# Kernel tuning notes

Hardware: AMD Instinct MI355X
Metric: run time of the kernel (lower is better)

The kernel has to match this reference:

```python
import jax, jax.numpy as jnp
import numpy as np

B, C, H, W = 8, 256, 128, 128


def setup_inputs() -> dict:
    key = jax.random.key(0)
    ks = jax.random.split(key, 8)
    s = 1.0 / np.sqrt(C)
    return {
        "edge_feature": jax.random.normal(ks[0], (B, C, H, W), jnp.float32),
        "mask_feature": jax.random.normal(ks[1], (B, C, H, W), jnp.float32),
        # 1x1 conv weights [out_dim, in_dim] + biases
        "Wq": jax.random.normal(ks[2], (C, C), jnp.float32) * s,
        "bq": jax.random.normal(ks[3], (C,), jnp.float32) * 0.01,
        "Wk": jax.random.normal(ks[4], (C, C), jnp.float32) * s,
        "bk": jax.random.normal(ks[5], (C,), jnp.float32) * 0.01,
        "Wv": jax.random.normal(ks[6], (C, C), jnp.float32) * s,
        "bv": jax.random.normal(ks[7], (C,), jnp.float32) * 0.01,
        # torch initializes gamma=0; use 0.5 so the attention path is exercised
        "gamma": jnp.array(0.5, jnp.float32),
    }


def _conv1x1(x, w, b):
    # x: [B,C,H,W], w: [O,C] -> [B,O,H,W]
    return jnp.einsum('oc,bchw->bohw', w, x) + b[None, :, None, None]


def reference(edge_feature, mask_feature, Wq, bq, Wk, bk, Wv, bv, gamma):
    b, c, h, w = edge_feature.shape
    q = _conv1x1(edge_feature, Wq, bq)
    k = _conv1x1(edge_feature, Wk, bk)
    v = _conv1x1(mask_feature, Wv, bv)

    # Criss-cross energies (note: source forward does NOT apply the INF diag mask)
    energy_H = jnp.einsum('bchw,bcjw->bhwj', q, k)  # [B,H,W,H] column attention
    energy_W = jnp.einsum('bchw,bchj->bhwj', q, k)  # [B,H,W,W] row attention

    att = jax.nn.softmax(jnp.concatenate([energy_H, energy_W], axis=3), axis=3)
    att_H4 = att[..., :h]   # [B,H,W,H]
    att_W4 = att[..., h:]   # [B,H,W,W]

    out_H = jnp.einsum('bcjw,bhwj->bchw', v, att_H4)
    out_W = jnp.einsum('bchj,bhwj->bchw', v, att_W4)
    out = gamma * (out_H + out_W) + mask_feature

    # Match torch's returned attention layouts: [B*W,H,H] and [B*H,W,W]
    att_H = jnp.transpose(att_H4, (0, 2, 1, 3)).reshape(b * w, h, h)
    att_W = att_W4.reshape(b * h, w, w)
    return (out, att_H, att_W)
```

## Files before the change

kernel.cpp:

```cpp
#include <hip/hip_runtime.h>

typedef unsigned short u16;
typedef unsigned int   u32;
typedef __attribute__((ext_vector_type(8))) short short8;
typedef __attribute__((ext_vector_type(4))) float f32x4;

#define HW_   16384
constexpr long CHW_ = 4194304L;
constexpr long NT   = 33554432L;

#define GLDS(g, l) __builtin_amdgcn_global_load_lds( \
    (const __attribute__((address_space(1))) void*)(g), \
    (__attribute__((address_space(3))) void*)(l), 16, 0, 0)

__device__ inline u16 f2bf(float x){ u32 u = __float_as_uint(x); u += 0x7fff + ((u>>16)&1); return (u16)(u>>16); }
__device__ inline float bf2f(u16 h){ return __uint_as_float(((u32)h)<<16); }

__device__ inline const short8* frg(const u16* T, int r, int c){
  return (const short8*)(T + r*64 + ((c ^ (r&7))<<3));
}


template<int MODE>
__global__ __launch_bounds__(256) void gemm_nt(
    const char* __restrict__ Aq, const char* __restrict__ Bq,
    const char* __restrict__ Aq2, const char* __restrict__ Bq2,
    const float* __restrict__ bias, const float* __restrict__ gammap,
    float* __restrict__ outFa, float* __restrict__ outFb,
    u16* __restrict__ outUa, u16* __restrict__ outUb)
{
  constexpr int NTl = (MODE <= 1) ? 8 : (MODE == 2 ? 4 : 2);
  __shared__ __align__(16) u16 smem[34048];

  const int t    = threadIdx.x;
  const int lane = t & 63;
  const int wid  = t >> 6;
  const int wr   = (wid >> 1) << 6;
  const int wc   = (wid & 1) << 6;

  long abase = 0, bbase = 0, ars = 0, brs = 0;
  int b = 0, m0 = 0, n0 = 0, xx = 0, ct = 0, dir = 0, sOut = 0;
  const char* Ause = Aq;
  const char* Buse = Bq;
  u16* outU = outUa;

  if constexpr (MODE == 0) {
    b = blockIdx.z; m0 = blockIdx.x << 7; n0 = blockIdx.y << 7;
    abase = ((long)b * HW_ + m0) * 1024; ars = 1024;
    bbase = (long)n0 * 1024;             brs = 1024;
  } else if constexpr (MODE == 1) {
    int bid = blockIdx.x;
    b = bid >> 8; dir = (bid >> 7) & 1; xx = bid & 127;
    sOut = b * 128 + xx;
    if (dir) { abase = (long)b * 16777216L + (long)xx * 1024; ars = 131072; }
    else     { abase = (long)b * 16777216L + (long)xx * 131072; ars = 1024; }
    bbase = abase; brs = ars;
  } else if constexpr (MODE == 2) {
    b = blockIdx.z; m0 = blockIdx.y << 7; n0 = blockIdx.x << 7;
    abase = (long)m0 * 512;              ars = 512;
    bbase = ((long)b * HW_ + n0) * 512;  brs = 512;
  } else {
    int s = blockIdx.x; ct = blockIdx.y; b = s >> 7; xx = s & 127;
    sOut = s;
    if (blockIdx.z) { Ause = Aq2; Buse = Bq2; outU = outUb; }
    abase = ((long)b * 256 + (long)(ct << 7)) * 32768L + (long)xx * 256; ars = 32768;
    bbase = (long)s * 32768L; brs = 256;
  }

  const char* pA = Ause + abase;
  const char* pB = Buse + bbase;

  f32x4 acc[4][4];
  for (int i = 0; i < 4; i++)
    for (int j = 0; j < 4; j++)
      acc[i][j] = (f32x4){0.f, 0.f, 0.f, 0.f};

  auto stage = [&](int buf, int kt) {
    u16* T1 = smem + buf * 17024;
    u16* T2 = T1 + 8192;
    const long ko = (long)kt * 128;
    #pragma unroll
    for (int i = 0; i < 4; i++) {
      int r = (i << 5) + (t >> 3);
      int c = (t & 7) ^ (r & 7);
      GLDS(pA + (long)r * ars + ko + (c << 4), T1 + (i << 11) + ((t >> 6) << 9));
      GLDS(pB + (long)r * brs + ko + (c << 4), T2 + (i << 11) + ((t >> 6) << 9));
    }
  };

  const int khi = lane >> 4;
  const int rl  = lane & 15;

  stage(0, 0);
  stage(1, 1);

  #pragma unroll
  for (int kt = 0; kt < NTl; ++kt) {
    if (kt + 1 < NTl) asm volatile("s_waitcnt vmcnt(8)" ::: "memory");
    else              asm volatile("s_waitcnt vmcnt(0)" ::: "memory");
    __builtin_amdgcn_sched_barrier(0);
    __builtin_amdgcn_s_barrier();
    __builtin_amdgcn_sched_barrier(0);

    const u16* T1 = smem + (kt & 1) * 17024;
    const u16* T2 = T1 + 8192;

    short8 fa0[4], fa1[4], fb0[4], fb1[4];
    #pragma unroll
    for (int f = 0; f < 4; f++) {
      fa0[f] = *frg(T1, wr + f * 16 + rl, khi);
      fa1[f] = *frg(T1, wr + f * 16 + rl, 4 + khi);
      fb0[f] = *frg(T2, wc + f * 16 + rl, khi);
      fb1[f] = *frg(T2, wc + f * 16 + rl, 4 + khi);
    }

    __builtin_amdgcn_s_setprio(1);
    #pragma unroll
    for (int fm = 0; fm < 4; fm++) {
      #pragma unroll
      for (int fn = 0; fn < 4; fn++) {
        if constexpr (MODE <= 1) {
          acc[fm][fn] = __builtin_amdgcn_mfma_f32_16x16x32_bf16(fa0[fm], fb0[fn], acc[fm][fn], 0, 0, 0);
          acc[fm][fn] = __builtin_amdgcn_mfma_f32_16x16x32_bf16(fa0[fm], fb1[fn], acc[fm][fn], 0, 0, 0);
          acc[fm][fn] = __builtin_amdgcn_mfma_f32_16x16x32_bf16(fa1[fm], fb0[fn], acc[fm][fn], 0, 0, 0);
        } else {
          acc[fm][fn] = __builtin_amdgcn_mfma_f32_16x16x32_bf16(fa0[fm], fb0[fn], acc[fm][fn], 0, 0, 0);
          acc[fm][fn] = __builtin_amdgcn_mfma_f32_16x16x32_bf16(fa1[fm], fb1[fn], acc[fm][fn], 0, 0, 0);
        }
      }
    }
    __builtin_amdgcn_s_setprio(0);

    __builtin_amdgcn_s_barrier();
    __builtin_amdgcn_sched_barrier(0);
    if (kt + 2 < NTl) stage(kt & 1, kt + 2);
  }

  float gma = 0.f;
  if constexpr (MODE == 3) gma = gammap[0];
  float* LDSE = (float*)smem;

  #pragma unroll
  for (int fm = 0; fm < 4; fm++) {
    #pragma unroll
    for (int fn = 0; fn < 4; fn++) {
      #pragma unroll
      for (int r = 0; r < 4; r++) {
        int lr = wr + fm * 16 + ((lane >> 4) << 2) + r;
        int lc = wc + fn * 16 + rl;
        float v = acc[fm][fn][r];
        if constexpr (MODE == 0) v += bias[n0 + lc];
        if constexpr (MODE == 2) v += bias[m0 + lr];
        if constexpr (MODE == 3) v *= gma;
        LDSE[lr * 132 + lc] = v;
      }
    }
  }
  __syncthreads();

  if constexpr (MODE == 0) {
    u16* outp = (n0 < 256) ? outUa : outUb;
    long rowb = ((long)b * HW_ + m0) * 512;
    int cbu = (n0 & 255) * 2;
    #pragma unroll
    for (int k = 0; k < 16; ++k) {
      int row = k * 8 + (t >> 5);
      int iu  = (t & 31) * 8;
      int off = iu & 63;
      int lcol = (iu >> 6) * 32 + (off & 31);
      const float* src = &LDSE[row * 132 + lcol];
      u16 o[8];
      if (off < 32) {
        #pragma unroll
        for (int j = 0; j < 8; j++) o[j] = f2bf(src[j]);
      } else {
        #pragma unroll
        for (int j = 0; j < 8; j++) { float v = src[j]; u16 h = f2bf(v); o[j] = f2bf(v - bf2f(h)); }
      }
      *(short8*)(outp + rowb + (long)row * 512 + cbu + iu) = *(short8*)o;
    }
  } else if constexpr (MODE == 1) {
    float* op = dir ? outFb : outFa;
    long ob = (long)sOut * 16384;
    #pragma unroll
    for (int k = 0; k < 16; ++k) {
      int row = k * 8 + (t >> 5);
      int c4 = (t & 31) * 4;
      f32x4 v = *(const f32x4*)&LDSE[row * 132 + c4];
      *(f32x4*)(op + ob + (long)row * 128 + c4) = v;
    }
  } else {
    #pragma unroll
    for (int k = 0; k < 8; ++k) {
      int row = k * 16 + (t >> 4);
      int c8 = (t & 15) * 8;
      const float* src = &LDSE[row * 132 + c8];
      u16 o[8];
      #pragma unroll
      for (int j = 0; j < 8; j++) o[j] = f2bf(src[j]);
      long addr;
      if constexpr (MODE == 2) addr = ((long)b * 256 + m0 + row) * HW_ + n0 + c8;
      else                     addr = ((long)b * 256 + (ct << 7) + row) * HW_ + (long)xx * 128 + c8;
      *(short8*)(outU + addr) = *(short8*)o;
    }
  }
}

__global__ __launch_bounds__(256) void split_transpose2(const float* __restrict__ edge,
    const float* __restrict__ mask, u16* __restrict__ Xs, u16* __restrict__ Mt)
{
  int b = blockIdx.z, c0 = blockIdx.y << 5, p0 = blockIdx.x << 5;
  __shared__ float tileE[32][33];
  __shared__ float tileM[32][33];
  int tx = threadIdx.x, ty = threadIdx.y;
  const float* E = edge + (long)b * CHW_;
  const float* M = mask + (long)b * CHW_;
  #pragma unroll
  for (int r = 0; r < 4; r++) {
    int cc = ty + (r << 3);
    long g = (long)(c0 + cc) * HW_ + p0 + tx;
    tileE[cc][tx] = E[g];
    tileM[cc][tx] = M[g];
  }
  __syncthreads();
  int blk = (c0 >> 5) * 64;
  #pragma unroll
  for (int r = 0; r < 4; r++) {
    int pp = ty + (r << 3);
    long prow = (long)b * HW_ + p0 + pp;
    float x = tileE[tx][pp];
    u16 h = f2bf(x);
    Xs[prow * 512 + blk + tx]      = h;
    Xs[prow * 512 + blk + 32 + tx] = f2bf(x - bf2f(h));
    Mt[prow * 256 + c0 + tx]       = f2bf(tileM[tx][pp]);
  }
}

__global__ __launch_bounds__(256) void wsplit(const float* __restrict__ Wq,
    const float* __restrict__ Wk, const float* __restrict__ Wv,
    const float* __restrict__ bq, const float* __restrict__ bk,
    u16* Wc, u16* Wvp, float* bcat)
{
  int i = blockIdx.x * 256 + threadIdx.x;
  int o = i >> 8, c = i & 255;
  long pos = (long)o * 512 + (c >> 5) * 64 + (c & 31);
  float q = Wq[i]; u16 a = f2bf(q); Wc[pos] = a; Wc[pos + 32] = f2bf(q - bf2f(a));
  float k = Wk[i]; u16 d = f2bf(k);
  Wc[pos + 131072] = d; Wc[pos + 131072 + 32] = f2bf(k - bf2f(d));
  Wvp[i] = f2bf(Wv[i]);
  if (blockIdx.x == 0) {
    bcat[threadIdx.x]       = bq[threadIdx.x];
    bcat[256 + threadIdx.x] = bk[threadIdx.x];
  }
}

__global__ __launch_bounds__(256) void transpose_hw_bf16(const u16* __restrict__ src,
                                                         u16* __restrict__ dst)
{
  int bc = blockIdx.z;
  int h0 = blockIdx.x << 5, w0 = blockIdx.y << 5;
  long base = (long)bc * HW_;
  __shared__ u16 tile[32][34];
  int tx = threadIdx.x, ty = threadIdx.y;
  #pragma unroll
  for (int r = 0; r < 4; r++)
    tile[ty + (r << 3)][tx] = src[base + (long)(h0 + ty + (r << 3)) * 128 + w0 + tx];
  __syncthreads();
  #pragma unroll
  for (int r = 0; r < 4; r++) {
    int ww = ty + (r << 3);
    dst[base + (long)(w0 + ww) * 128 + h0 + tx] = tile[tx][ww];
  }
}

__global__ __launch_bounds__(256) void softmax_kernel(float* __restrict__ attH,
    float* __restrict__ attW, u16* __restrict__ aHb, u16* __restrict__ aWb)
{
  int g  = threadIdx.x & 31;
  long r = (long)blockIdx.x * 8 + (threadIdx.x >> 5);
  int b = (int)(r >> 14);
  int h = (int)((r >> 7) & 127);
  int w = (int)(r & 127);
  long baseH = ((long)(b * 128 + w) * 128 + h) * 128;
  long baseW = r * 128;
  float* rp = (g < 16) ? (attH + baseH) : (attW + baseW);
  u16*   up = (g < 16) ? (aHb + baseH)  : (aWb + baseW);
  int j0 = (g & 15) * 8;
  f32x4 v0 = *(f32x4*)(rp + j0);
  f32x4 v1 = *(f32x4*)(rp + j0 + 4);
  float m = fmaxf(fmaxf(fmaxf(v0.x, v0.y), fmaxf(v0.z, v0.w)),
                  fmaxf(fmaxf(v1.x, v1.y), fmaxf(v1.z, v1.w)));
  #pragma unroll
  for (int off = 16; off; off >>= 1) m = fmaxf(m, __shfl_xor(m, off, 32));
  float e[8];
  e[0]=expf(v0.x-m); e[1]=expf(v0.y-m); e[2]=expf(v0.z-m); e[3]=expf(v0.w-m);
  e[4]=expf(v1.x-m); e[5]=expf(v1.y-m); e[6]=expf(v1.z-m); e[7]=expf(v1.w-m);
  float s = ((e[0]+e[1])+(e[2]+e[3])) + ((e[4]+e[5])+(e[6]+e[7]));
  #pragma unroll
  for (int off = 16; off; off >>= 1) s += __shfl_xor(s, off, 32);
  float inv = 1.0f / s;
  #pragma unroll
  for (int j = 0; j < 8; j++) e[j] *= inv;
  __builtin_nontemporal_store((f32x4){e[0], e[1], e[2], e[3]}, (f32x4*)(rp + j0));
  __builtin_nontemporal_store((f32x4){e[4], e[5], e[6], e[7]}, (f32x4*)(rp + j0 + 4));
  u16 o[8];
  #pragma unroll
  for (int j = 0; j < 8; j++) o[j] = f2bf(e[j]);
  *(short8*)(up + j0) = *(short8*)o;
}

__global__ __launch_bounds__(256) void merge_kernel(const u16* __restrict__ tmp,
    const u16* __restrict__ pW, const float* __restrict__ mask, float* __restrict__ out)
{
  int bc = blockIdx.z;
  int h0 = blockIdx.x << 5, w0 = blockIdx.y << 5;
  long base = (long)bc * HW_;
  __shared__ u16 tile[32][33];
  int tx = threadIdx.x, ty = threadIdx.y;
  #pragma unroll
  for (int r = 0; r < 4; r++) {
    int ww = ty + (r << 3);
    tile[ww][tx] = tmp[base + (long)(w0 + ww) * 128 + h0 + tx];
  }
  __syncthreads();
  #pragma unroll
  for (int r = 0; r < 4; r++) {
    int hh = ty + (r << 3);
    long o = base + (long)(h0 + hh) * 128 + w0 + tx;
    float v = bf2f(pW[o]) + bf2f(tile[tx][hh]) + mask[o];
    __builtin_nontemporal_store(v, out + o);
  }
}

extern "C" void kernel_launch(void* const* d_in, const int* in_sizes, int n_in,
                              void* d_out, int out_size, void* d_ws, size_t ws_size,
                              hipStream_t stream) {
  const float* edge  = (const float*)d_in[0];
  const float* mask  = (const float*)d_in[1];
  const float* Wq    = (const float*)d_in[2];
  const float* bq    = (const float*)d_in[3];
  const float* Wk    = (const float*)d_in[4];
  const float* bk    = (const float*)d_in[5];
  const float* Wv    = (const float*)d_in[6];
  const float* bv    = (const float*)d_in[7];
  const float* gamma = (const float*)d_in[8];

  float* out  = (float*)d_out;
  float* attH = out + NT;
  float* attW = attH + 16777216L;

  char* W = (char*)d_ws;
  u16* Xs  = (u16*)(W);
  u16* Mt  = (u16*)(W + 134217728L);
  u16* Qs  = (u16*)(W + 201326592L);
  u16* Ks  = (u16*)(W + 335544320L);
  u16* Vb  = (u16*)(W + 469762048L);
  u16* Wc  = (u16*)(W + 536870912L);
  u16* Wvp = Wc + 262144;
  float* bcat = (float*)(Wvp + 65536);
  u16* Vtb = (u16*)(W);
  u16* aWb = (u16*)(W + 67108864L);
  u16* aHb = (u16*)(W + 100663296L);
  u16* tmp = (u16*)(W + 201326592L);
  u16* pW  = (u16*)(W + 335544320L);

  dim3 tb(32, 8);

  wsplit<<<256, 256, 0, stream>>>(Wq, Wk, Wv, bq, bk, Wc, Wvp, bcat);
  split_transpose2<<<dim3(512, 8, 8), tb, 0, stream>>>(edge, mask, Xs, Mt);

  gemm_nt<0><<<dim3(128, 4, 8), 256, 0, stream>>>(
      (const char*)Xs, (const char*)Wc, nullptr, nullptr, bcat, nullptr,
      nullptr, nullptr, Qs, Ks);
  gemm_nt<2><<<dim3(128, 2, 8), 256, 0, stream>>>(
      (const char*)Wvp, (const char*)Mt, nullptr, nullptr, bv, nullptr,
      nullptr, nullptr, Vb, nullptr);

  transpose_hw_bf16<<<dim3(4, 4, 2048), tb, 0, stream>>>(Vb, Vtb);

  gemm_nt<1><<<dim3(2048), 256, 0, stream>>>(
      (const char*)Qs, (const char*)Ks, nullptr, nullptr, nullptr, nullptr,
      attW, attH, nullptr, nullptr);

  softmax_kernel<<<dim3(16384), 256, 0, stream>>>(attH, attW, aHb, aWb);

  gemm_nt<3><<<dim3(1024, 2, 2), 256, 0, stream>>>(
      (const char*)Vtb, (const char*)aHb, (const char*)Vb, (const char*)aWb,
      nullptr, gamma, nullptr, nullptr, tmp, pW);

  merge_kernel<<<dim3(4, 4, 2048), tb, 0, stream>>>(tmp, pW, mask, out);
}
```

Baseline: 623.1 us.

## Shrink GEMM LDS footprint, add XCD-aware block swizzle and two-pass epilogue

Non-split GEMM modes now stage 64-wide K tiles with a new 4-column swizzle, which halves their LDS buffer so more blocks fit per CU. Launch bounds now request higher occupancy. All GEMM grids are flattened to 1D and remapped so consecutive blocks spread across the 8 XCDs. The epilogue writes its LDS staging in two 64-row passes so it fits in the smaller shared buffer. This trades more K iterations and extra barriers for better occupancy and cache locality.

```diff
diff --git a/kernel.cpp b/kernel.cpp
--- a/kernel.cpp
+++ b/kernel.cpp
@@ -16,21 +16,26 @@
 __device__ inline u16 f2bf(float x){ u32 u = __float_as_uint(x); u += 0x7fff + ((u>>16)&1); return (u16)(u>>16); }
 __device__ inline float bf2f(u16 h){ return __uint_as_float(((u32)h)<<16); }
 
-__device__ inline const short8* frg(const u16* T, int r, int c){
+__device__ inline const short8* frgS(const u16* T, int r, int c){
   return (const short8*)(T + r*64 + ((c ^ (r&7))<<3));
 }
-
+__device__ inline const short8* frgP(const u16* T, int r, int c){
+  return (const short8*)(T + r*32 + ((c ^ (r&3) ^ (((r>>2)&1)<<1))<<3));
+}
 
 template<int MODE>
-__global__ __launch_bounds__(256) void gemm_nt(
+__global__ __launch_bounds__(256, (MODE <= 1) ? 2 : 4) void gemm_nt(
     const char* __restrict__ Aq, const char* __restrict__ Bq,
     const char* __restrict__ Aq2, const char* __restrict__ Bq2,
     const float* __restrict__ bias, const float* __restrict__ gammap,
     float* __restrict__ outFa, float* __restrict__ outFb,
     u16* __restrict__ outUa, u16* __restrict__ outUb)
 {
-  constexpr int NTl = (MODE <= 1) ? 8 : (MODE == 2 ? 4 : 2);
-  __shared__ __align__(16) u16 smem[34048];
+  constexpr bool SP   = (MODE <= 1);
+  constexpr int  NTl  = (MODE == 3) ? 4 : 8;
+  constexpr int  BUFU = SP ? 16384 : 8192;
+  constexpr int  LDSU = SP ? 32768 : 16896;
+  __shared__ __align__(16) u16 smem[LDSU];
 
   const int t    = threadIdx.x;
   const int lane = t & 63;
@@ -45,24 +50,31 @@
   u16* outU = outUa;
 
   if constexpr (MODE == 0) {
-    b = blockIdx.z; m0 = blockIdx.x << 7; n0 = blockIdx.y << 7;
+    int bid = blockIdx.x;
+    int orig = (bid & 7) * 512 + (bid >> 3);
+    b = orig >> 9; m0 = ((orig >> 2) & 127) << 7; n0 = (orig & 3) << 7;
     abase = ((long)b * HW_ + m0) * 1024; ars = 1024;
     bbase = (long)n0 * 1024;             brs = 1024;
   } else if constexpr (MODE == 1) {
     int bid = blockIdx.x;
-    b = bid >> 8; dir = (bid >> 7) & 1; xx = bid & 127;
+    int orig = (bid & 7) * 256 + (bid >> 3);
+    b = orig >> 8; dir = (orig >> 7) & 1; xx = orig & 127;
     sOut = b * 128 + xx;
     if (dir) { abase = (long)b * 16777216L + (long)xx * 1024; ars = 131072; }
     else     { abase = (long)b * 16777216L + (long)xx * 131072; ars = 1024; }
     bbase = abase; brs = ars;
   } else if constexpr (MODE == 2) {
-    b = blockIdx.z; m0 = blockIdx.y << 7; n0 = blockIdx.x << 7;
+    int bid = blockIdx.x;
+    int orig = (bid & 7) * 256 + (bid >> 3);
+    b = orig >> 8; m0 = (orig & 1) << 7; n0 = ((orig >> 1) & 127) << 7;
     abase = (long)m0 * 512;              ars = 512;
     bbase = ((long)b * HW_ + n0) * 512;  brs = 512;
   } else {
-    int s = blockIdx.x; ct = blockIdx.y; b = s >> 7; xx = s & 127;
-    sOut = s;
-    if (blockIdx.z) { Ause = Aq2; Buse = Bq2; outU = outUb; }
+    int bid = blockIdx.x;
+    int orig = (bid & 7) * 512 + (bid >> 3);
+    ct = orig & 1; int s = (orig >> 1) & 1023; int z = orig >> 11;
+    b = s >> 7; xx = s & 127; sOut = s;
+    if (z) { Ause = Aq2; Buse = Bq2; outU = outUb; }
     abase = ((long)b * 256 + (long)(ct << 7)) * 32768L + (long)xx * 256; ars = 32768;
     bbase = (long)s * 32768L; brs = 256;
   }
@@ -76,13 +88,19 @@
       acc[i][j] = (f32x4){0.f, 0.f, 0.f, 0.f};
 
   auto stage = [&](int buf, int kt) {
-    u16* T1 = smem + buf * 17024;
-    u16* T2 = T1 + 8192;
-    const long ko = (long)kt * 128;
+    u16* T1 = smem + buf * BUFU;
+    u16* T2 = T1 + BUFU / 2;
+    const long ko = (long)kt * (SP ? 128 : 64);
     #pragma unroll
-    for (int i = 0; i < 4; i++) {
-      int r = (i << 5) + (t >> 3);
-      int c = (t & 7) ^ (r & 7);
+    for (int i = 0; i < (SP ? 4 : 2); i++) {
+      int r, c;
+      if constexpr (SP) {
+        r = (i << 5) + (t >> 3);
+        c = (t & 7) ^ (r & 7);
+      } else {
+        r = (i << 6) + (t >> 2);
+        c = (t & 3) ^ (r & 3) ^ (((r >> 2) & 1) << 1);
+      }
       GLDS(pA + (long)r * ars + ko + (c << 4), T1 + (i << 11) + ((t >> 6) << 9));
       GLDS(pB + (long)r * brs + ko + (c << 4), T2 + (i << 11) + ((t >> 6) << 9));
     }
@@ -96,40 +114,54 @@
 
   #pragma unroll
   for (int kt = 0; kt < NTl; ++kt) {
-    if (kt + 1 < NTl) asm volatile("s_waitcnt vmcnt(8)" ::: "memory");
-    else              asm volatile("s_waitcnt vmcnt(0)" ::: "memory");
+    if (kt + 1 < NTl) {
+      if constexpr (SP) asm volatile("s_waitcnt vmcnt(8)" ::: "memory");
+      else              asm volatile("s_waitcnt vmcnt(4)" ::: "memory");
+    } else {
+      asm volatile("s_waitcnt vmcnt(0)" ::: "memory");
+    }
     __builtin_amdgcn_sched_barrier(0);
     __builtin_amdgcn_s_barrier();
     __builtin_amdgcn_sched_barrier(0);
 
-    const u16* T1 = smem + (kt & 1) * 17024;
-    const u16* T2 = T1 + 8192;
-
-    short8 fa0[4], fa1[4], fb0[4], fb1[4];
-    #pragma unroll
-    for (int f = 0; f < 4; f++) {
-      fa0[f] = *frg(T1, wr + f * 16 + rl, khi);
-      fa1[f] = *frg(T1, wr + f * 16 + rl, 4 + khi);
-      fb0[f] = *frg(T2, wc + f * 16 + rl, khi);
-      fb1[f] = *frg(T2, wc + f * 16 + rl, 4 + khi);
-    }
-
-    __builtin_amdgcn_s_setprio(1);
-    #pragma unroll
-    for (int fm = 0; fm < 4; fm++) {
-      #pragma unroll
-      for (int fn = 0; fn < 4; fn++) {
-        if constexpr (MODE <= 1) {
+    const u16* T1 = smem + (kt & 1) * BUFU;
+    const u16* T2 = T1 + BUFU / 2;
+
+    if constexpr (SP) {
+      short8 fa0[4], fa1[4], fb0[4], fb1[4];
+      #pragma unroll
+      for (int f = 0; f < 4; f++) {
+        fa0[f] = *frgS(T1, wr + f * 16 + rl, khi);
+        fa1[f] = *frgS(T1, wr + f * 16 + rl, 4 + khi);
+        fb0[f] = *frgS(T2, wc + f * 16 + rl, khi);
+        fb1[f] = *frgS(T2, wc + f * 16 + rl, 4 + khi);
+      }
+      __builtin_amdgcn_s_setprio(1);
+      #pragma unroll
+      for (int fm = 0; fm < 4; fm++) {
+        #pragma unroll
+        for (int fn = 0; fn < 4; fn++) {
           acc[fm][fn] = __builtin_amdgcn_mfma_f32_16x16x32_bf16(fa0[fm], fb0[fn], acc[fm][fn], 0, 0, 0);
           acc[fm][fn] = __builtin_amdgcn_mfma_f32_16x16x32_bf16(fa0[fm], fb1[fn], acc[fm][fn], 0, 0, 0);
           acc[fm][fn] = __builtin_amdgcn_mfma_f32_16x16x32_bf16(fa1[fm], fb0[fn], acc[fm][fn], 0, 0, 0);
-        } else {
-          acc[fm][fn] = __builtin_amdgcn_mfma_f32_16x16x32_bf16(fa0[fm], fb0[fn], acc[fm][fn], 0, 0, 0);
-          acc[fm][fn] = __builtin_amdgcn_mfma_f32_16x16x32_bf16(fa1[fm], fb1[fn], acc[fm][fn], 0, 0, 0);
         }
       }
+      __builtin_amdgcn_s_setprio(0);
+    } else {
+      short8 fa[4], fb[4];
+      #pragma unroll
+      for (int f = 0; f < 4; f++) {
+        fa[f] = *frgP(T1, wr + f * 16 + rl, khi);
+        fb[f] = *frgP(T2, wc + f * 16 + rl, khi);
+      }
+      __builtin_amdgcn_s_setprio(1);
+      #pragma unroll
+      for (int fm = 0; fm < 4; fm++)
+        #pragma unroll
+        for (int fn = 0; fn < 4; fn++)
+          acc[fm][fn] = __builtin_amdgcn_mfma_f32_16x16x32_bf16(fa[fm], fb[fn], acc[fm][fn], 0, 0, 0);
+      __builtin_amdgcn_s_setprio(0);
     }
-    __builtin_amdgcn_s_setprio(0);
 
     __builtin_amdgcn_s_barrier();
     __builtin_amdgcn_sched_barrier(0);
@@ -141,67 +173,76 @@
   float* LDSE = (float*)smem;
 
   #pragma unroll
-  for (int fm = 0; fm < 4; fm++) {
-    #pragma unroll
-    for (int fn = 0; fn < 4; fn++) {
-      #pragma unroll
-      for (int r = 0; r < 4; r++) {
-        int lr = wr + fm * 16 + ((lane >> 4) << 2) + r;
-        int lc = wc + fn * 16 + rl;
-        float v = acc[fm][fn][r];
-        if constexpr (MODE == 0) v += bias[n0 + lc];
-        if constexpr (MODE == 2) v += bias[m0 + lr];
-        if constexpr (MODE == 3) v *= gma;
-        LDSE[lr * 132 + lc] = v;
+  for (int pass = 0; pass < 2; ++pass) {
+    if (pass) __syncthreads();
+    if ((wid >> 1) == pass) {
+      #pragma unroll
+      for (int fm = 0; fm < 4; fm++) {
+        #pragma unroll
+        for (int fn = 0; fn < 4; fn++) {
+          #pragma unroll
+          for (int r = 0; r < 4; r++) {
+            int Lr = fm * 16 + ((lane >> 4) << 2) + r;
+            int lc = wc + fn * 16 + rl;
+            float v = acc[fm][fn][r];
+            if constexpr (MODE == 0) v += bias[n0 + lc];
+            if constexpr (MODE == 2) v += bias[m0 + pass * 64 + Lr];
+            if constexpr (MODE == 3) v *= gma;
+            LDSE[Lr * 132 + lc] = v;
+          }
+        }
       }
     }
-  }
-  __syncthreads();
-
-  if constexpr (MODE == 0) {
-    u16* outp = (n0 < 256) ? outUa : outUb;
-    long rowb = ((long)b * HW_ + m0) * 512;
-    int cbu = (n0 & 255) * 2;
-    #pragma unroll
-    for (int k = 0; k < 16; ++k) {
-      int row = k * 8 + (t >> 5);
-      int iu  = (t & 31) * 8;
-      int off = iu & 63;
-      int lcol = (iu >> 6) * 32 + (off & 31);
-      const float* src = &LDSE[row * 132 + lcol];
-      u16 o[8];
-      if (off < 32) {
+    __syncthreads();
+
+    if constexpr (MODE == 0) {
+      u16* outp = (n0 < 256) ? outUa : outUb;
+      long rowb = ((long)b * HW_ + m0) * 512;
+      int cbu = (n0 & 255) * 2;
+      #pragma unroll
+      for (int k = 0; k < 8; ++k) {
+        int Lr = k * 8 + (t >> 5);
+        int row = pass * 64 + Lr;
+        int iu  = (t & 31) * 8;
+        int off = iu & 63;
+        int lcol = (iu >> 6) * 32 + (off & 31);
+        const float* src = &LDSE[Lr * 132 + lcol];
+        u16 o[8];
+        if (off < 32) {
+          #pragma unroll
+          for (int j = 0; j < 8; j++) o[j] = f2bf(src[j]);
+        } else {
+          #pragma unroll
+          for (int j = 0; j < 8; j++) { float v = src[j]; u16 h = f2bf(v); o[j] = f2bf(v - bf2f(h)); }
+        }
+        *(short8*)(outp + rowb + (long)row * 512 + cbu + iu) = *(short8*)o;
+      }
+    } else if constexpr (MODE == 1) {
+      float* op = dir ? outFb : outFa;
+      long ob = (long)sOut * 16384;
+      #pragma unroll
+      for (int k = 0; k < 8; ++k) {
+        int Lr = k * 8 + (t >> 5);
+        int row = pass * 64 + Lr;
+        int c4 = (t & 31) * 4;
+        f32x4 v = *(const f32x4*)&LDSE[Lr * 132 + c4];
+        *(f32x4*)(op + ob + (long)row * 128 + c4) = v;
+      }
+    } else {
+      #pragma unroll
+      for (int k = 0; k < 4; ++k) {
+        int Lr = k * 16 + (t >> 4);
+        int row = pass * 64 + Lr;
+        int c8 = (t & 15) * 8;
+        const float* src = &LDSE[Lr * 132 + c8];
+        u16 o[8];
         #pragma unroll
         for (int j = 0; j < 8; j++) o[j] = f2bf(src[j]);
-      } else {
-        #pragma unroll
-        for (int j = 0; j < 8; j++) { float v = src[j]; u16 h = f2bf(v); o[j] = f2bf(v - bf2f(h)); }
-      }
-      *(short8*)(outp + rowb + (long)row * 512 + cbu + iu) = *(short8*)o;
-    }
-  } else if constexpr (MODE == 1) {
-    float* op = dir ? outFb : outFa;
-    long ob = (long)sOut * 16384;
-    #pragma unroll
-    for (int k = 0; k < 16; ++k) {
-      int row = k * 8 + (t >> 5);
-      int c4 = (t & 31) * 4;
-      f32x4 v = *(const f32x4*)&LDSE[row * 132 + c4];
-      *(f32x4*)(op + ob + (long)row * 128 + c4) = v;
-    }
-  } else {
-    #pragma unroll
-    for (int k = 0; k < 8; ++k) {
-      int row = k * 16 + (t >> 4);
-      int c8 = (t & 15) * 8;
-      const float* src = &LDSE[row * 132 + c8];
-      u16 o[8];
-      #pragma unroll
-      for (int j = 0; j < 8; j++) o[j] = f2bf(src[j]);
-      long addr;
-      if constexpr (MODE == 2) addr = ((long)b * 256 + m0 + row) * HW_ + n0 + c8;
-      else                     addr = ((long)b * 256 + (ct << 7) + row) * HW_ + (long)xx * 128 + c8;
-      *(short8*)(outU + addr) = *(short8*)o;
+        long addr;
+        if constexpr (MODE == 2) addr = ((long)b * 256 + m0 + row) * HW_ + n0 + c8;
+        else                     addr = ((long)b * 256 + (ct << 7) + row) * HW_ + (long)xx * 128 + c8;
+        *(short8*)(outU + addr) = *(short8*)o;
+      }
     }
   }
 }
@@ -369,22 +410,22 @@
   wsplit<<<256, 256, 0, stream>>>(Wq, Wk, Wv, bq, bk, Wc, Wvp, bcat);
   split_transpose2<<<dim3(512, 8, 8), tb, 0, stream>>>(edge, mask, Xs, Mt);
 
-  gemm_nt<0><<<dim3(128, 4, 8), 256, 0, stream>>>(
+  gemm_nt<0><<<4096, 256, 0, stream>>>(
       (const char*)Xs, (const char*)Wc, nullptr, nullptr, bcat, nullptr,
       nullptr, nullptr, Qs, Ks);
-  gemm_nt<2><<<dim3(128, 2, 8), 256, 0, stream>>>(
+  gemm_nt<2><<<2048, 256, 0, stream>>>(
       (const char*)Wvp, (const char*)Mt, nullptr, nullptr, bv, nullptr,
       nullptr, nullptr, Vb, nullptr);
 
   transpose_hw_bf16<<<dim3(4, 4, 2048), tb, 0, stream>>>(Vb, Vtb);
 
-  gemm_nt<1><<<dim3(2048), 256, 0, stream>>>(
+  gemm_nt<1><<<2048, 256, 0, stream>>>(
       (const char*)Qs, (const char*)Ks, nullptr, nullptr, nullptr, nullptr,
       attW, attH, nullptr, nullptr);
 
-  softmax_kernel<<<dim3(16384), 256, 0, stream>>>(attH, attW, aHb, aWb);
-
-  gemm_nt<3><<<dim3(1024, 2, 2), 256, 0, stream>>>(
+  softmax_kernel<<<16384, 256, 0, stream>>>(attH, attW, aHb, aWb);
+
+  gemm_nt<3><<<4096, 256, 0, stream>>>(
       (const char*)Vtb, (const char*)aHb, (const char*)Vb, (const char*)aWb,
       nullptr, gamma, nullptr, nullptr, tmp, pW);
 
```

Measured after the change: 677.4 us. +8.7%, slower.

## Single-buffer GEMM LDS and split epilogue to raise occupancy, remap MODE0 blocks

Applied to the files above, without the earlier changes.

The GEMM kernel drops its double-buffered LDS (about 68KB) for a single buffer (about 34KB) and sets launch bounds to 4 blocks per CU. To fit, the epilogue stages results through LDS in two half passes. The MODE 0 projection GEMM also moves to a 1D grid with an interleaved block-to-tile mapping, aiming for better L2 reuse across batches. The aim is to hide latency with more resident blocks, at the cost of losing the software prefetch pipeline. Each k-step now waits on its own loads, plus extra barriers.

```diff
diff --git a/kernel.cpp b/kernel.cpp
--- a/kernel.cpp
+++ b/kernel.cpp
@@ -20,17 +20,17 @@
   return (const short8*)(T + r*64 + ((c ^ (r&7))<<3));
 }
 
-
 template<int MODE>
-__global__ __launch_bounds__(256) void gemm_nt(
+__global__ __launch_bounds__(256, 4) void gemm_nt(
     const char* __restrict__ Aq, const char* __restrict__ Bq,
     const char* __restrict__ Aq2, const char* __restrict__ Bq2,
     const float* __restrict__ bias, const float* __restrict__ gammap,
     float* __restrict__ outFa, float* __restrict__ outFb,
     u16* __restrict__ outUa, u16* __restrict__ outUb)
 {
-  constexpr int NTl = (MODE <= 1) ? 8 : (MODE == 2 ? 4 : 2);
-  __shared__ __align__(16) u16 smem[34048];
+  constexpr bool SP  = (MODE <= 1);
+  constexpr int  NTl = SP ? 8 : (MODE == 2 ? 4 : 2);
+  __shared__ __align__(16) u16 smem[16896];
 
   const int t    = threadIdx.x;
   const int lane = t & 63;
@@ -45,7 +45,9 @@
   u16* outU = outUa;
 
   if constexpr (MODE == 0) {
-    b = blockIdx.z; m0 = blockIdx.x << 7; n0 = blockIdx.y << 7;
+    int bid = blockIdx.x;
+    int orig = (bid & 7) * 512 + (bid >> 3);
+    b = orig >> 9; m0 = ((orig >> 2) & 127) << 7; n0 = (orig & 3) << 7;
     abase = ((long)b * HW_ + m0) * 1024; ars = 1024;
     bbase = (long)n0 * 1024;             brs = 1024;
   } else if constexpr (MODE == 1) {
@@ -75,65 +77,68 @@
     for (int j = 0; j < 4; j++)
       acc[i][j] = (f32x4){0.f, 0.f, 0.f, 0.f};
 
-  auto stage = [&](int buf, int kt) {
-    u16* T1 = smem + buf * 17024;
-    u16* T2 = T1 + 8192;
-    const long ko = (long)kt * 128;
-    #pragma unroll
-    for (int i = 0; i < 4; i++) {
-      int r = (i << 5) + (t >> 3);
-      int c = (t & 7) ^ (r & 7);
-      GLDS(pA + (long)r * ars + ko + (c << 4), T1 + (i << 11) + ((t >> 6) << 9));
-      GLDS(pB + (long)r * brs + ko + (c << 4), T2 + (i << 11) + ((t >> 6) << 9));
-    }
-  };
-
   const int khi = lane >> 4;
   const int rl  = lane & 15;
 
-  stage(0, 0);
-  stage(1, 1);
-
   #pragma unroll
   for (int kt = 0; kt < NTl; ++kt) {
-    if (kt + 1 < NTl) asm volatile("s_waitcnt vmcnt(8)" ::: "memory");
-    else              asm volatile("s_waitcnt vmcnt(0)" ::: "memory");
-    __builtin_amdgcn_sched_barrier(0);
-    __builtin_amdgcn_s_barrier();
-    __builtin_amdgcn_sched_barrier(0);
-
-    const u16* T1 = smem + (kt & 1) * 17024;
-    const u16* T2 = T1 + 8192;
-
-    short8 fa0[4], fa1[4], fb0[4], fb1[4];
-    #pragma unroll
-    for (int f = 0; f < 4; f++) {
-      fa0[f] = *frg(T1, wr + f * 16 + rl, khi);
-      fa1[f] = *frg(T1, wr + f * 16 + rl, 4 + khi);
-      fb0[f] = *frg(T2, wc + f * 16 + rl, khi);
-      fb1[f] = *frg(T2, wc + f * 16 + rl, 4 + khi);
+    {
+      const long ko = (long)kt * 128;
+      #pragma unroll
+      for (int i = 0; i < 4; i++) {
+        int r = (i << 5) + (t >> 3);
+        int c = (t & 7) ^ (r & 7);
+        GLDS(pA + (long)r * ars + ko + (c << 4), smem + (i << 11) + ((t >> 6) << 9));
+        GLDS(pB + (long)r * brs + ko + (c << 4), smem + 8192 + (i << 11) + ((t >> 6) << 9));
+      }
     }
-
-    __builtin_amdgcn_s_setprio(1);
-    #pragma unroll
-    for (int fm = 0; fm < 4; fm++) {
-      #pragma unroll
-      for (int fn = 0; fn < 4; fn++) {
-        if constexpr (MODE <= 1) {
+    __syncthreads();
+
+    const u16* T1 = smem;
+    const u16* T2 = smem + 8192;
+
+    if constexpr (SP) {
+      short8 fa0[4], fa1[4], fb0[4], fb1[4];
+      #pragma unroll
+      for (int f = 0; f < 4; f++) {
+        fa0[f] = *frg(T1, wr + f * 16 + rl, khi);
+        fa1[f] = *frg(T1, wr + f * 16 + rl, 4 + khi);
+        fb0[f] = *frg(T2, wc + f * 16 + rl, khi);
+        fb1[f] = *frg(T2, wc + f * 16 + rl, 4 + khi);
+      }
+      __builtin_amdgcn_s_setprio(1);
+      #pragma unroll
+      for (int fm = 0; fm < 4; fm++) {
+        #pragma unroll
+        for (int fn = 0; fn < 4; fn++) {
           acc[fm][fn] = __builtin_amdgcn_mfma_f32_16x16x32_bf16(fa0[fm], fb0[fn], acc[fm][fn], 0, 0, 0);
           acc[fm][fn] = __builtin_amdgcn_mfma_f32_16x16x32_bf16(fa0[fm], fb1[fn], acc[fm][fn], 0, 0, 0);
           acc[fm][fn] = __builtin_amdgcn_mfma_f32_16x16x32_bf16(fa1[fm], fb0[fn], acc[fm][fn], 0, 0, 0);
-        } else {
+        }
+      }
+      __builtin_amdgcn_s_setprio(0);
+    } else {
+      short8 fa0[4], fa1[4], fb0[4], fb1[4];
+      #pragma unroll
+      for (int f = 0; f < 4; f++) {
+        fa0[f] = *frg(T1, wr + f * 16 + rl, khi);
+        fa1[f] = *frg(T1, wr + f * 16 + rl, 4 + khi);
+        fb0[f] = *frg(T2, wc + f * 16 + rl, khi);
+        fb1[f] = *frg(T2, wc + f * 16 + rl, 4 + khi);
+      }
+      __builtin_amdgcn_s_setprio(1);
+      #pragma unroll
+      for (int fm = 0; fm < 4; fm++) {
+        #pragma unroll
+        for (int fn = 0; fn < 4; fn++) {
           acc[fm][fn] = __builtin_amdgcn_mfma_f32_16x16x32_bf16(fa0[fm], fb0[fn], acc[fm][fn], 0, 0, 0);
           acc[fm][fn] = __builtin_amdgcn_mfma_f32_16x16x32_bf16(fa1[fm], fb1[fn], acc[fm][fn], 0, 0, 0);
         }
       }
+      __builtin_amdgcn_s_setprio(0);
     }
-    __builtin_amdgcn_s_setprio(0);
-
-    __builtin_amdgcn_s_barrier();
-    __builtin_amdgcn_sched_barrier(0);
-    if (kt + 2 < NTl) stage(kt & 1, kt + 2);
+
+    __syncthreads();
   }
 
   float gma = 0.f;
@@ -141,67 +146,76 @@
   float* LDSE = (float*)smem;
 
   #pragma unroll
-  for (int fm = 0; fm < 4; fm++) {
-    #pragma unroll
-    for (int fn = 0; fn < 4; fn++) {
-      #pragma unroll
-      for (int r = 0; r < 4; r++) {
-        int lr = wr + fm * 16 + ((lane >> 4) << 2) + r;
-        int lc = wc + fn * 16 + rl;
-        float v = acc[fm][fn][r];
-        if constexpr (MODE == 0) v += bias[n0 + lc];
-        if constexpr (MODE == 2) v += bias[m0 + lr];
-        if constexpr (MODE == 3) v *= gma;
-        LDSE[lr * 132 + lc] = v;
+  for (int pass = 0; pass < 2; ++pass) {
+    if (pass) __syncthreads();
+    if ((wid >> 1) == pass) {
+      #pragma unroll
+      for (int fm = 0; fm < 4; fm++) {
+        #pragma unroll
+        for (int fn = 0; fn < 4; fn++) {
+          #pragma unroll
+          for (int r = 0; r < 4; r++) {
+            int Lr = fm * 16 + ((lane >> 4) << 2) + r;
+            int lc = wc + fn * 16 + rl;
+            float v = acc[fm][fn][r];
+            if constexpr (MODE == 0) v += bias[n0 + lc];
+            if constexpr (MODE == 2) v += bias[m0 + pass * 64 + Lr];
+            if constexpr (MODE == 3) v *= gma;
+            LDSE[Lr * 132 + lc] = v;
+          }
+        }
       }
     }
-  }
-  __syncthreads();
-
-  if constexpr (MODE == 0) {
-    u16* outp = (n0 < 256) ? outUa : outUb;
-    long rowb = ((long)b * HW_ + m0) * 512;
-    int cbu = (n0 & 255) * 2;
-    #pragma unroll
-    for (int k = 0; k < 16; ++k) {
-      int row = k * 8 + (t >> 5);
-      int iu  = (t & 31) * 8;
-      int off = iu & 63;
-      int lcol = (iu >> 6) * 32 + (off & 31);
-      const float* src = &LDSE[row * 132 + lcol];
-      u16 o[8];
-      if (off < 32) {
+    __syncthreads();
+
+    if constexpr (MODE == 0) {
+      u16* outp = (n0 < 256) ? outUa : outUb;
+      long rowb = ((long)b * HW_ + m0) * 512;
+      int cbu = (n0 & 255) * 2;
+      #pragma unroll
+      for (int k = 0; k < 8; ++k) {
+        int Lr = k * 8 + (t >> 5);
+        int row = pass * 64 + Lr;
+        int iu  = (t & 31) * 8;
+        int off = iu & 63;
+        int lcol = (iu >> 6) * 32 + (off & 31);
+        const float* src = &LDSE[Lr * 132 + lcol];
+        u16 o[8];
+        if (off < 32) {
+          #pragma unroll
+          for (int j = 0; j < 8; j++) o[j] = f2bf(src[j]);
+        } else {
+          #pragma unroll
+          for (int j = 0; j < 8; j++) { float v = src[j]; u16 h = f2bf(v); o[j] = f2bf(v - bf2f(h)); }
+        }
+        *(short8*)(outp + rowb + (long)row * 512 + cbu + iu) = *(short8*)o;
+      }
+    } else if constexpr (MODE == 1) {
+      float* op = dir ? outFb : outFa;
+      long ob = (long)sOut * 16384;
+      #pragma unroll
+      for (int k = 0; k < 8; ++k) {
+        int Lr = k * 8 + (t >> 5);
+        int row = pass * 64 + Lr;
+        int c4 = (t & 31) * 4;
+        f32x4 v = *(const f32x4*)&LDSE[Lr * 132 + c4];
+        *(f32x4*)(op + ob + (long)row * 128 + c4) = v;
+      }
+    } else {
+      #pragma unroll
+      for (int k = 0; k < 4; ++k) {
+        int Lr = k * 16 + (t >> 4);
+        int row = pass * 64 + Lr;
+        int c8 = (t & 15) * 8;
+        const float* src = &LDSE[Lr * 132 + c8];
+        u16 o[8];
         #pragma unroll
         for (int j = 0; j < 8; j++) o[j] = f2bf(src[j]);
-      } else {
-        #pragma unroll
-        for (int j = 0; j < 8; j++) { float v = src[j]; u16 h = f2bf(v); o[j] = f2bf(v - bf2f(h)); }
-      }
-      *(short8*)(outp + rowb + (long)row * 512 + cbu + iu) = *(short8*)o;
-    }
-  } else if constexpr (MODE == 1) {
-    float* op = dir ? outFb : outFa;
-    long ob = (long)sOut * 16384;
-    #pragma unroll
-    for (int k = 0; k < 16; ++k) {
-      int row = k * 8 + (t >> 5);
-      int c4 = (t & 31) * 4;
-      f32x4 v = *(const f32x4*)&LDSE[row * 132 + c4];
-      *(f32x4*)(op + ob + (long)row * 128 + c4) = v;
-    }
-  } else {
-    #pragma unroll
-    for (int k = 0; k < 8; ++k) {
-      int row = k * 16 + (t >> 4);
-      int c8 = (t & 15) * 8;
-      const float* src = &LDSE[row * 132 + c8];
-      u16 o[8];
-      #pragma unroll
-      for (int j = 0; j < 8; j++) o[j] = f2bf(src[j]);
-      long addr;
-      if constexpr (MODE == 2) addr = ((long)b * 256 + m0 + row) * HW_ + n0 + c8;
-      else                     addr = ((long)b * 256 + (ct << 7) + row) * HW_ + (long)xx * 128 + c8;
-      *(short8*)(outU + addr) = *(short8*)o;
+        long addr;
+        if constexpr (MODE == 2) addr = ((long)b * 256 + m0 + row) * HW_ + n0 + c8;
+        else                     addr = ((long)b * 256 + (ct << 7) + row) * HW_ + (long)xx * 128 + c8;
+        *(short8*)(outU + addr) = *(short8*)o;
+      }
     }
   }
 }
@@ -369,7 +383,7 @@
   wsplit<<<256, 256, 0, stream>>>(Wq, Wk, Wv, bq, bk, Wc, Wvp, bcat);
   split_transpose2<<<dim3(512, 8, 8), tb, 0, stream>>>(edge, mask, Xs, Mt);
 
-  gemm_nt<0><<<dim3(128, 4, 8), 256, 0, stream>>>(
+  gemm_nt<0><<<4096, 256, 0, stream>>>(
       (const char*)Xs, (const char*)Wc, nullptr, nullptr, bcat, nullptr,
       nullptr, nullptr, Qs, Ks);
   gemm_nt<2><<<dim3(128, 2, 8), 256, 0, stream>>>(
@@ -378,11 +392,11 @@
 
   transpose_hw_bf16<<<dim3(4, 4, 2048), tb, 0, stream>>>(Vb, Vtb);
 
-  gemm_nt<1><<<dim3(2048), 256, 0, stream>>>(
+  gemm_nt<1><<<2048, 256, 0, stream>>>(
       (const char*)Qs, (const char*)Ks, nullptr, nullptr, nullptr, nullptr,
       attW, attH, nullptr, nullptr);
 
-  softmax_kernel<<<dim3(16384), 256, 0, stream>>>(attH, attW, aHb, aWb);
+  softmax_kernel<<<16384, 256, 0, stream>>>(attH, attW, aHb, aWb);
 
   gemm_nt<3><<<dim3(1024, 2, 2), 256, 0, stream>>>(
       (const char*)Vtb, (const char*)aHb, (const char*)Vb, (const char*)aWb,
```

After: 1.123 ms. 80.3% more time.
